# Kernel optimization log

Hardware: AMD Instinct MI355X
Metric: run time of the kernel (lower is better)

## Reference

```python
import jax, jax.numpy as jnp
import numpy as np
from jax import lax

B, NMEAS, M, LAYER_NUM = 2048, 128, 256, 10
CLAMP_MIN, CLAMP_MAX = 1e-6, 100.0
EPS_S = 1e-6


def _conv2d(x, w, b):
    y = lax.conv_general_dilated(x, w, (1, 1), 'SAME', dimension_numbers=('NCHW', 'OIHW', 'NCHW'))
    return y + b[None, :, None, None]


def _conv1d(x, w, b):
    y = lax.conv_general_dilated(x, w, (1,), 'SAME', dimension_numbers=('NCH', 'OIH', 'NCH'))
    return y + b[None, :, None]


def setup_inputs():
    key = jax.random.key(0)
    ks = jax.random.split(key, 12)
    s = 1.0 / np.sqrt(2.0 * NMEAS)  # ~unit-norm dictionary columns
    return {
        'Yr': jax.random.normal(ks[0], (B, 1, NMEAS, 1), jnp.float32),
        'Yi': jax.random.normal(ks[1], (B, 1, NMEAS, 1), jnp.float32),
        'Ar': s * jax.random.normal(ks[2], (NMEAS, M), jnp.float32),
        'Ai': s * jax.random.normal(ks[3], (NMEAS, M), jnp.float32),
        'conv1_w': 0.1 * jax.random.normal(ks[4], (32, 2, 3, 3), jnp.float32),
        'conv1_b': jnp.zeros((32,), jnp.float32),
        'conv2_w': 0.1 * jax.random.normal(ks[5], (64, 32, 3, 3), jnp.float32),
        'conv2_b': jnp.zeros((64,), jnp.float32),
        'hc_w': 0.1 * jax.random.normal(ks[6], (LAYER_NUM - 1, 64, 3), jnp.float32),
        'hc_b': jnp.zeros((LAYER_NUM - 1,), jnp.float32),
        'hd_w': 0.1 * jax.random.normal(ks[7], (LAYER_NUM - 1, 64, 3), jnp.float32),
        'hd_b': jnp.zeros((LAYER_NUM - 1,), jnp.float32),
        'hT_w': 0.1 * jax.random.normal(ks[8], (LAYER_NUM, 64, 3), jnp.float32),
        'hT_b': jnp.zeros((LAYER_NUM,), jnp.float32),
        'a0': jnp.asarray(1.0, jnp.float32),
        'b0': jnp.asarray(1.0, jnp.float32),
    }


def _hypernet(ay, c1w, c1b, c2w, c2b, hcw, hcb, hdw, hdb, hTw, hTb):
    # ay: [B, 2, M]; batch acts as image width (context)
    x_img = jnp.transpose(ay, (1, 2, 0))[None]              # [1, 2, M, B]
    f = jax.nn.relu(_conv2d(x_img, c1w, c1b))               # [1, 32, M, B]
    f = jax.nn.relu(_conv2d(f, c2w, c2b))                   # [1, 64, M, B]
    f = jnp.mean(f, axis=2)                                 # AdaptiveAvgPool2d((1,None)) -> [1, 64, B]
    c = jnp.abs(_conv1d(f, hcw, hcb))[0].T                  # [B, L-1]
    d = jnp.abs(_conv1d(f, hdw, hdb))[0].T                  # [B, L-1]
    T = jnp.abs(_conv1d(f, hTw, hTb))[0].T                  # [B, L]
    c = jnp.clip(c, CLAMP_MIN, CLAMP_MAX)
    d = jnp.maximum(d, CLAMP_MIN)
    T = jnp.clip(T, CLAMP_MIN, CLAMP_MAX)
    return c, d, T


def _forward(Yr, Yi, Ar, Ai, conv1_w, conv1_b, conv2_w, conv2_b,
             hc_w, hc_b, hd_w, hd_b, hT_w, hT_b, a0, b0):
    Y = (Yr + 1j * Yi).astype(jnp.complex64)                # [B,1,Nmeas,1]
    A = (Ar + 1j * Ai).astype(jnp.complex64)                # [Nmeas,M]
    AT = A.conj().T                                         # [M,Nmeas]
    AA = AT @ A                                             # [M,M] Hermitian
    AY = jnp.matmul(AT, Y)                                  # [B,1,M,1]
    b = Y.shape[0]
    n = Y.shape[2]
    ay = jnp.concatenate([AY.real.reshape(b, 1, -1), AY.imag.reshape(b, 1, -1)], axis=1)  # [B,2,M]
    c, d, T = _hypernet(ay, conv1_w, conv1_b, conv2_w, conv2_b,
                        hc_w, hc_b, hd_w, hd_b, hT_w, hT_b)
    D = jnp.real(jnp.diagonal(AA))[None, None, :, None]     # diag of Hermitian AA is real; [1,1,M,1]
    eps = (a0 / b0).astype(jnp.complex64) * jnp.ones((b, 1, 1, 1), jnp.complex64)
    Lam = ((c[:, 0] / d[:, 0])[:, None, None, None] * jnp.ones((1, 1, M, 1), jnp.float32)).astype(jnp.complex64)
    U = jnp.zeros((b, 1, M, 1), jnp.complex64)
    a = a0 + n
    for k in range(LAYER_NUM - 1):
        Tk = T[:, k][:, None, None, None]
        # fused SBL/VAMP mean update
        U = eps * (Tk * U - jnp.matmul(AA, U) + AY) / (eps * Tk + Lam + EPS_S)
        Sigma = 1.0 / (eps * D + Lam + EPS_S)
        r = Y - jnp.matmul(A, U)
        eps1 = jnp.sum(r.real ** 2 + r.imag ** 2, axis=(2, 3), keepdims=True)  # ||.||_F^2
        eps2 = jnp.sum(D * Sigma, axis=(2, 3), keepdims=True)
        eps = a / (b0 + eps1 + eps2 + EPS_S)
        Lam = (c[:, k][:, None, None, None] + 1.0) / (
            d[:, k][:, None, None, None] + jnp.abs(U) ** 2 + Sigma + EPS_S)
    Tk = T[:, LAYER_NUM - 1][:, None, None, None]
    U = eps * (Tk * U - jnp.matmul(AA, U) + AY) / (eps * Tk + Lam + EPS_S)
    Ua = jnp.abs(U)
    Ua = Ua / (jnp.max(Ua) + 1e-8)
    return Ua, c, d, T


def reference(Yr, Yi, Ar, Ai, conv1_w, conv1_b, conv2_w, conv2_b,
              hc_w, hc_b, hd_w, hd_b, hT_w, hT_b, a0, b0):
    Ua, c, d, T = _forward(Yr, Yi, Ar, Ai, conv1_w, conv1_b, conv2_w, conv2_b,
                           hc_w, hc_b, hd_w, hd_b, hT_w, hT_b, a0, b0)
    # original returns the last batch row of c/d/T (detached diagnostics)
    return Ua, c[-1:, :], d[-1:, :], T[-1:, :]
```

## Files before the change

kernel.cpp:

```cpp
#include <hip/hip_runtime.h>
#include <math.h>

#define B_N   2048
#define NM    128
#define M_N   256
#define LNUM  10
#define EPS_Sf 1e-6f

typedef _Float16 half8 __attribute__((ext_vector_type(8)));
typedef float floatx4 __attribute__((ext_vector_type(4)));

static constexpr size_t o_AA  = 0;
static constexpr size_t o_D   = o_AA  + 131072;
static constexpr size_t o_yn  = o_D   + 256;
static constexpr size_t o_AY  = o_yn  + 2048;
static constexpr size_t o_AYt = o_AY  + 1048576;
static constexpr size_t o_w2t = o_AYt + 1048576;
static constexpr size_t o_z1  = o_w2t + 18432;
static constexpr size_t o_fp  = o_z1  + 16777216;
static constexpr size_t o_f   = o_fp  + 2097152;
static constexpr size_t o_c   = o_f   + 131072;
static constexpr size_t o_dd  = o_c   + 18432;
static constexpr size_t o_T   = o_dd  + 18432;
static constexpr size_t o_Ua  = o_T   + 20480;
static constexpr size_t o_gm  = o_Ua  + 524288;

#define Z1T_RS (2050 * 32)

__device__ __forceinline__ void split2(float x, _Float16& h, _Float16& l) {
    h = (_Float16)x;
    l = (_Float16)(x - (float)h);
}

__global__ void k_aa(const float* __restrict__ Ar, const float* __restrict__ Ai,
                     float* __restrict__ ws) {
    __shared__ float cr[NM], ci[NM];
    int i = blockIdx.x, j = threadIdx.x;
    if (j < NM) { cr[j] = Ar[j * M_N + i]; ci[j] = Ai[j * M_N + i]; }
    __syncthreads();
    float sr = 0.f, si = 0.f;
    for (int n = 0; n < NM; ++n) {
        float ar = Ar[n * M_N + j], ai = Ai[n * M_N + j];
        sr += cr[n] * ar + ci[n] * ai;
        si += cr[n] * ai - ci[n] * ar;
    }
    _Float16* A16 = (_Float16*)(ws + o_AA);
    size_t off = ((size_t)((i >> 4) * 8 + (j >> 5)) * 64
                  + (size_t)(((j >> 3) & 3) * 16 + (i & 15))) * 8 + (j & 7);
    A16[off]         = (_Float16)sr;
    A16[65536 + off] = (_Float16)si;
    if (j == i) ws[o_D + i] = sr;
}

__global__ void k_w2t(const float* __restrict__ w2, float* __restrict__ ws) {
    int i = blockIdx.x * 256 + threadIdx.x;
    if (i < 64 * 32 * 9) {
        int oc = i / 288, r = i % 288;
        int ic = r / 9, kk = r % 9;
        _Float16* Wa = (_Float16*)(ws + o_w2t);
        Wa[((size_t)oc * 9 + kk) * 32 + ic] = (_Float16)w2[i];
    }
}

__global__ void k_ay(const float* __restrict__ Yr, const float* __restrict__ Yi,
                     const float* __restrict__ Ar, const float* __restrict__ Ai,
                     float* __restrict__ ws) {
    __shared__ float2 Ys[8][NM];
    int bb0 = blockIdx.x * 8;
    int tid = threadIdx.x;
    for (int i = tid; i < 8 * NM; i += 256) {
        int g = i >> 7, n = i & 127;
        Ys[g][n] = make_float2(Yr[(size_t)(bb0 + g) * NM + n], Yi[(size_t)(bb0 + g) * NM + n]);
    }
    __syncthreads();
    if (tid < 8) {
        float s = 0.f;
        for (int n = 0; n < NM; ++n) { float2 y = Ys[tid][n]; s += y.x * y.x + y.y * y.y; }
        ws[o_yn + bb0 + tid] = s;
    }
    int m = tid;
    float accr[8], acci[8];
#pragma unroll
    for (int g = 0; g < 8; ++g) { accr[g] = 0.f; acci[g] = 0.f; }
    for (int n = 0; n < NM; ++n) {
        float ar = Ar[n * M_N + m], ai = Ai[n * M_N + m];
#pragma unroll
        for (int g = 0; g < 8; ++g) {
            float2 y = Ys[g][n];
            accr[g] += ar * y.x + ai * y.y;
            acci[g] += ar * y.y - ai * y.x;
        }
    }
    float2* AY = (float2*)(ws + o_AY);
#pragma unroll
    for (int g = 0; g < 8; ++g) {
        AY[(size_t)(bb0 + g) * M_N + m] = make_float2(accr[g], acci[g]);
        ws[o_AYt + (size_t)m * B_N + (bb0 + g)] = accr[g];
        ws[o_AYt + 524288 + (size_t)m * B_N + (bb0 + g)] = acci[g];
    }
}

__global__ void k_conv1(const float* __restrict__ w1, const float* __restrict__ b1,
                        float* __restrict__ ws) {
    __shared__ float w1s[576], b1s[32];
    int tid = threadIdx.x;
    for (int i = tid; i < 576; i += 256) w1s[i] = w1[i];
    if (tid < 32) b1s[tid] = b1[tid];
    __syncthreads();
    int gidx = blockIdx.x * 256 + tid;
    int b = gidx & (B_N - 1), m = gidx >> 11;
    const float* xr = ws + o_AYt;
    float x[2][3][3];
#pragma unroll
    for (int c = 0; c < 2; ++c)
#pragma unroll
        for (int dm = 0; dm < 3; ++dm) {
            int mm = m + dm - 1;
#pragma unroll
            for (int db = 0; db < 3; ++db) {
                int bb = b + db - 1;
                x[c][dm][db] = (mm >= 0 && mm < M_N && bb >= 0 && bb < B_N)
                                 ? xr[(size_t)c * 524288 + (size_t)mm * B_N + bb] : 0.f;
            }
        }
    _Float16* z1t = (_Float16*)(ws + o_z1);
    _Float16 zv[32];
    for (int oc = 0; oc < 32; ++oc) {
        float acc = b1s[oc];
#pragma unroll
        for (int c = 0; c < 2; ++c)
#pragma unroll
            for (int dm = 0; dm < 3; ++dm)
#pragma unroll
                for (int db = 0; db < 3; ++db)
                    acc += x[c][dm][db] * w1s[oc * 18 + c * 9 + dm * 3 + db];
        zv[oc] = (_Float16)fmaxf(acc, 0.f);
    }
    _Float16* dst = z1t + (size_t)(m + 1) * Z1T_RS + (size_t)(b + 1) * 32;
#pragma unroll
    for (int v = 0; v < 4; ++v) *(half8*)(dst + v * 8) = *(half8*)(zv + v * 8);
    half8 z8 = (half8)((_Float16)0.f);
    if (m == 0) {
        _Float16* d2 = z1t + (size_t)(b + 1) * 32;
#pragma unroll
        for (int v = 0; v < 4; ++v) *(half8*)(d2 + v * 8) = z8;
        if (b == 0) { _Float16* d3 = z1t;
#pragma unroll
            for (int v = 0; v < 4; ++v) *(half8*)(d3 + v * 8) = z8; }
        if (b == B_N - 1) { _Float16* d3 = z1t + (size_t)2049 * 32;
#pragma unroll
            for (int v = 0; v < 4; ++v) *(half8*)(d3 + v * 8) = z8; }
    }
    if (m == M_N - 1) {
        _Float16* d2 = z1t + (size_t)257 * Z1T_RS + (size_t)(b + 1) * 32;
#pragma unroll
        for (int v = 0; v < 4; ++v) *(half8*)(d2 + v * 8) = z8;
        if (b == 0) { _Float16* d3 = z1t + (size_t)257 * Z1T_RS;
#pragma unroll
            for (int v = 0; v < 4; ++v) *(half8*)(d3 + v * 8) = z8; }
        if (b == B_N - 1) { _Float16* d3 = z1t + (size_t)257 * Z1T_RS + (size_t)2049 * 32;
#pragma unroll
            for (int v = 0; v < 4; ++v) *(half8*)(d3 + v * 8) = z8; }
    }
    if (b == 0) {
        _Float16* d2 = z1t + (size_t)(m + 1) * Z1T_RS;
#pragma unroll
        for (int v = 0; v < 4; ++v) *(half8*)(d2 + v * 8) = z8;
    }
    if (b == B_N - 1) {
        _Float16* d2 = z1t + (size_t)(m + 1) * Z1T_RS + (size_t)2049 * 32;
#pragma unroll
        for (int v = 0; v < 4; ++v) *(half8*)(d2 + v * 8) = z8;
    }
}

#define MFMA16(A,Bv,C) C = __builtin_amdgcn_mfma_f32_16x16x32_f16(A, Bv, C, 0, 0, 0)
__global__ void __launch_bounds__(128)
k_conv2m(const float* __restrict__ b2, float* __restrict__ ws) {
    int tid = threadIdx.x;
    int lane = tid & 63, wv = tid >> 6;
    int col = lane & 15, quad = lane >> 4;
    int bt = blockIdx.x & 127, g = blockIdx.x >> 7;
    int b0 = bt * 16, m0 = g * 16;
    int oc0w = wv * 32;
    const _Float16* z1t = (const _Float16*)(ws + o_z1);
    const _Float16* Wa  = (const _Float16*)(ws + o_w2t);

    half8 Af[2][9];
#pragma unroll
    for (int t = 0; t < 2; ++t)
#pragma unroll
        for (int kk = 0; kk < 9; ++kk)
            Af[t][kk] = *(const half8*)(Wa + ((size_t)(oc0w + t * 16 + col) * 9 + kk) * 32 + quad * 8);
    float bias[2][4];
#pragma unroll
    for (int t = 0; t < 2; ++t)
#pragma unroll
        for (int r = 0; r < 4; ++r)
            bias[t][r] = b2[oc0w + t * 16 + quad * 4 + r];

    const _Float16* zb = z1t + (size_t)(b0 + col) * 32 + quad * 8;
    half8 Bf[3][3];
#pragma unroll
    for (int ph = 0; ph < 3; ++ph)
#pragma unroll
        for (int db = 0; db < 3; ++db)
            Bf[ph][db] = *(const half8*)(zb + (size_t)(m0 + ph) * Z1T_RS + (size_t)db * 32);

    floatx4 facc[2];
    facc[0] = (floatx4){0.f, 0.f, 0.f, 0.f};
    facc[1] = (floatx4){0.f, 0.f, 0.f, 0.f};

#pragma unroll
    for (int mm = 0; mm < 16; ++mm) {
        floatx4 a0 = (floatx4){0.f, 0.f, 0.f, 0.f};
        floatx4 a1 = (floatx4){0.f, 0.f, 0.f, 0.f};
#pragma unroll
        for (int dm = 0; dm < 3; ++dm) {
            int ph = (mm + dm) % 3;
#pragma unroll
            for (int db = 0; db < 3; ++db) {
                MFMA16(Af[0][dm * 3 + db], Bf[ph][db], a0);
                MFMA16(Af[1][dm * 3 + db], Bf[ph][db], a1);
            }
        }
#pragma unroll
        for (int r = 0; r < 4; ++r) {
            facc[0][r] += fmaxf(a0[r] + bias[0][r], 0.f);
            facc[1][r] += fmaxf(a1[r] + bias[1][r], 0.f);
        }
        if (mm < 15) {
            int ph = mm % 3;
#pragma unroll
            for (int db = 0; db < 3; ++db)
                Bf[ph][db] = *(const half8*)(zb + (size_t)(m0 + mm + 3) * Z1T_RS + (size_t)db * 32);
        }
    }
    float* fp = ws + o_fp + (size_t)g * 131072;
#pragma unroll
    for (int t = 0; t < 2; ++t)
#pragma unroll
        for (int r = 0; r < 4; ++r)
            fp[(size_t)(oc0w + t * 16 + quad * 4 + r) * B_N + b0 + col] = facc[t][r];
}

__global__ void k_fred(float* __restrict__ ws) {
    size_t i = (size_t)blockIdx.x * 256 + threadIdx.x;
    float s = 0.f;
    for (int p = 0; p < 16; ++p) s += ws[o_fp + (size_t)p * 131072 + i];
    ws[o_f + i] = s * (1.f / 256.f);
}

__global__ void k_cdt(const float* __restrict__ hcw, const float* __restrict__ hcb,
                      const float* __restrict__ hdw, const float* __restrict__ hdb,
                      const float* __restrict__ hTw, const float* __restrict__ hTb,
                      float* __restrict__ ws, float* __restrict__ out) {
    int l = blockIdx.x >> 3;
    int b = (blockIdx.x & 7) * 256 + threadIdx.x;
    const float* f = ws + o_f;
    const float* w; float bi; int li, kind;
    if (l < 9)       { kind = 0; li = l;      w = hcw + (size_t)li * 192; bi = hcb[li]; }
    else if (l < 18) { kind = 1; li = l - 9;  w = hdw + (size_t)li * 192; bi = hdb[li]; }
    else             { kind = 2; li = l - 18; w = hTw + (size_t)li * 192; bi = hTb[li]; }
    __shared__ float wsm[192];
    for (int i = threadIdx.x; i < 192; i += 256) wsm[i] = w[i];
    __syncthreads();
    float acc = bi;
    bool okL = (b > 0), okR = (b < B_N - 1);
    for (int ic = 0; ic < 64; ++ic) {
        const float* fr = f + (size_t)ic * B_N + b;
        float fm1 = okL ? fr[-1] : 0.f;
        float f0  = fr[0];
        float fp1 = okR ? fr[1] : 0.f;
        acc += fm1 * wsm[ic * 3] + f0 * wsm[ic * 3 + 1] + fp1 * wsm[ic * 3 + 2];
    }
    float v = fmaxf(fabsf(acc), 1e-6f);
    if (kind != 1) v = fminf(v, 100.f);
    if (kind == 0)      { ws[o_c  + (size_t)b * 9  + li] = v; if (b == B_N - 1) out[524288 + li] = v; }
    else if (kind == 1) { ws[o_dd + (size_t)b * 9  + li] = v; if (b == B_N - 1) out[524297 + li] = v; }
    else                { ws[o_T  + (size_t)b * 10 + li] = v; if (b == B_N - 1) out[524306 + li] = v; }
}

__global__ void __launch_bounds__(1024, 4)
k_iter(const float* __restrict__ a0p, const float* __restrict__ b0p, float* __restrict__ ws) {
    __shared__ __align__(16) _Float16 Ubf[4][8][64][8];
    __shared__ float redv[16][16][3];
    __shared__ float redm[16];
    int tid = threadIdx.x;
    int lane = tid & 63, w = tid >> 6;
    int col = lane & 15, quad = lane >> 4;
    int b = blockIdx.x * 16 + col;
    const float2* AY = (const float2*)(ws + o_AY);
    const _Float16* Af = (const _Float16*)(ws + o_AA);
    float a0 = a0p[0], b0v = b0p[0];
    float atot = a0 + (float)NM;
    float yn = ws[o_yn + b];
    float eps = a0 / b0v;
    float lam0 = ws[o_c + (size_t)b * 9] / ws[o_dd + (size_t)b * 9];
    half8 Ar8[8], Ai8[8];
#pragma unroll
    for (int ks = 0; ks < 8; ++ks) {
        const _Float16* ab = Af + ((size_t)(w * 8 + ks) * 64 + lane) * 8;
        Ar8[ks] = *(const half8*)(ab);
        Ai8[ks] = *(const half8*)(ab + 65536);
    }
    float Dv[4], ayr[4], ayi[4], lam[4], Ur[4], Ui[4], sg[4], wr_[4], wi_[4];
#pragma unroll
    for (int r = 0; r < 4; ++r) {
        int m = w * 16 + quad * 4 + r;
        Dv[r] = ws[o_D + m];
        float2 a = AY[(size_t)b * M_N + m];
        ayr[r] = a.x; ayi[r] = a.y;
        lam[r] = lam0;
        Ur[r] = 0.f; Ui[r] = 0.f; wr_[r] = 0.f; wi_[r] = 0.f;
    }
    int ksw = w >> 1;
    int quadD = (w & 1) * 2 + (quad >> 1);
    int laneD = quadD * 16 + col;
    int eb = (quad & 1) * 4;
    for (int k = 0; k < LNUM; ++k) {
        float Tk = ws[o_T + (size_t)b * 10 + k];
#pragma unroll
        for (int r = 0; r < 4; ++r) {
            float iv = eps / (eps * Tk + lam[r] + EPS_Sf);
            Ur[r] = iv * (Tk * Ur[r] - wr_[r] + ayr[r]);
            Ui[r] = iv * (Tk * Ui[r] - wi_[r] + ayi[r]);
        }
        if (k == LNUM - 1) break;
        {
            union { _Float16 h[4]; unsigned long long u; } c0, c1, c2, c3;
#pragma unroll
            for (int r = 0; r < 4; ++r) {
                _Float16 h, l;
                split2(Ur[r], h, l); c0.h[r] = h; c1.h[r] = l;
                split2(Ui[r], h, l); c2.h[r] = h; c3.h[r] = l;
            }
            *(unsigned long long*)&Ubf[0][ksw][laneD][eb] = c0.u;
            *(unsigned long long*)&Ubf[1][ksw][laneD][eb] = c1.u;
            *(unsigned long long*)&Ubf[2][ksw][laneD][eb] = c2.u;
            *(unsigned long long*)&Ubf[3][ksw][laneD][eb] = c3.u;
        }
        __syncthreads();
        floatx4 wrp = (floatx4){0.f, 0.f, 0.f, 0.f};
        floatx4 wrn = (floatx4){0.f, 0.f, 0.f, 0.f};
        floatx4 wia = (floatx4){0.f, 0.f, 0.f, 0.f};
#pragma unroll
        for (int ks = 0; ks < 8; ++ks) {
            half8 urh = *(const half8*)&Ubf[0][ks][lane][0];
            half8 url = *(const half8*)&Ubf[1][ks][lane][0];
            half8 uih = *(const half8*)&Ubf[2][ks][lane][0];
            half8 uil = *(const half8*)&Ubf[3][ks][lane][0];
            MFMA16(Ar8[ks], urh, wrp);
            MFMA16(Ar8[ks], url, wrp);
            MFMA16(Ai8[ks], uih, wrn);
            MFMA16(Ai8[ks], uil, wrn);
            MFMA16(Ar8[ks], uih, wia);
            MFMA16(Ar8[ks], uil, wia);
            MFMA16(Ai8[ks], urh, wia);
            MFMA16(Ai8[ks], url, wia);
        }
        float p1 = 0.f, p2 = 0.f, p3 = 0.f;
#pragma unroll
        for (int r = 0; r < 4; ++r) {
            wr_[r] = wrp[r] - wrn[r];
            wi_[r] = wia[r];
            sg[r] = 1.f / (eps * Dv[r] + lam[r] + EPS_Sf);
            p1 += ayr[r] * Ur[r] + ayi[r] * Ui[r];
            p2 += Ur[r] * wr_[r] + Ui[r] * wi_[r];
            p3 += Dv[r] * sg[r];
        }
        p1 += __shfl_xor(p1, 16); p1 += __shfl_xor(p1, 32);
        p2 += __shfl_xor(p2, 16); p2 += __shfl_xor(p2, 32);
        p3 += __shfl_xor(p3, 16); p3 += __shfl_xor(p3, 32);
        if (lane < 16) { redv[w][col][0] = p1; redv[w][col][1] = p2; redv[w][col][2] = p3; }
        __syncthreads();
        float s1 = 0.f, s2 = 0.f, s3 = 0.f;
#pragma unroll
        for (int u16 = 0; u16 < 16; ++u16) {
            s1 += redv[u16][col][0]; s2 += redv[u16][col][1]; s3 += redv[u16][col][2];
        }
        float eps1 = fmaxf(yn - 2.f * s1 + s2, 0.f);
        eps = atot / (b0v + eps1 + s3 + EPS_Sf);
        float ck = ws[o_c + (size_t)b * 9 + k];
        float dk = ws[o_dd + (size_t)b * 9 + k];
#pragma unroll
        for (int r = 0; r < 4; ++r)
            lam[r] = (ck + 1.f) / (dk + Ur[r] * Ur[r] + Ui[r] * Ui[r] + sg[r] + EPS_Sf);
    }
    float4 v;
    v.x = sqrtf(Ur[0] * Ur[0] + Ui[0] * Ui[0]);
    v.y = sqrtf(Ur[1] * Ur[1] + Ui[1] * Ui[1]);
    v.z = sqrtf(Ur[2] * Ur[2] + Ui[2] * Ui[2]);
    v.w = sqrtf(Ur[3] * Ur[3] + Ui[3] * Ui[3]);
    *(float4*)&ws[o_Ua + (size_t)b * M_N + w * 16 + quad * 4] = v;
    float lm = fmaxf(fmaxf(v.x, v.y), fmaxf(v.z, v.w));
#pragma unroll
    for (int off = 32; off >= 1; off >>= 1) lm = fmaxf(lm, __shfl_xor(lm, off));
    if (lane == 0) redm[w] = lm;
    __syncthreads();
    if (tid == 0) {
        float mx = redm[0];
#pragma unroll
        for (int i = 1; i < 16; ++i) mx = fmaxf(mx, redm[i]);
        atomicMax((unsigned int*)(ws + o_gm), __float_as_uint(mx));
    }
}

__global__ void k_norm(const float* __restrict__ ws, float* __restrict__ out) {
    size_t i = (size_t)blockIdx.x * 256 + threadIdx.x;
    float gm = __uint_as_float(*(const unsigned int*)(ws + o_gm));
    out[i] = ws[o_Ua + i] / (gm + 1e-8f);
}

extern "C" void kernel_launch(void* const* d_in, const int* in_sizes, int n_in,
                              void* d_out, int out_size, void* d_ws, size_t ws_size,
                              hipStream_t stream) {
    (void)in_sizes; (void)n_in; (void)out_size; (void)ws_size;
    const float* Yr  = (const float*)d_in[0];
    const float* Yi  = (const float*)d_in[1];
    const float* Ar  = (const float*)d_in[2];
    const float* Ai  = (const float*)d_in[3];
    const float* w1  = (const float*)d_in[4];
    const float* b1  = (const float*)d_in[5];
    const float* w2  = (const float*)d_in[6];
    const float* b2  = (const float*)d_in[7];
    const float* hcw = (const float*)d_in[8];
    const float* hcb = (const float*)d_in[9];
    const float* hdw = (const float*)d_in[10];
    const float* hdb = (const float*)d_in[11];
    const float* hTw = (const float*)d_in[12];
    const float* hTb = (const float*)d_in[13];
    const float* a0  = (const float*)d_in[14];
    const float* b0  = (const float*)d_in[15];
    float* ws = (float*)d_ws;
    float* out = (float*)d_out;

    hipMemsetAsync((char*)d_ws + o_gm * sizeof(float), 0, 4, stream);
    k_aa    <<<256, 256, 0, stream>>>(Ar, Ai, ws);
    k_w2t   <<<72, 256, 0, stream>>>(w2, ws);
    k_ay    <<<256, 256, 0, stream>>>(Yr, Yi, Ar, Ai, ws);
    k_conv1 <<<2048, 256, 0, stream>>>(w1, b1, ws);
    k_conv2m<<<2048, 128, 0, stream>>>(b2, ws);
    k_fred  <<<512, 256, 0, stream>>>(ws);
    k_cdt   <<<224, 256, 0, stream>>>(hcw, hcb, hdw, hdb, hTw, hTb, ws, out);
    k_iter  <<<128, 1024, 0, stream>>>(a0, b0, ws);
    k_norm  <<<2048, 256, 0, stream>>>(ws, out);
}
```

Measured before the change: 244.2 us.

## Drop fp16 hi/lo split in iteration matvec and merge preprocessing kernels

The iterative solver kernel now converts U to a single fp16 value instead of a hi/lo fp16 pair. This halves the shared-memory staging and the MFMA count per step, at the cost of lower precision in the AA·U product. The three setup kernels and the workspace memset are merged into one block-partitioned launch to cut launch overhead. The cross-wave reduction buffer is transposed so each column reads its partial sums with vector loads.

```diff
diff --git a/kernel.cpp b/kernel.cpp
--- a/kernel.cpp
+++ b/kernel.cpp
@@ -27,76 +27,72 @@
 
 #define Z1T_RS (2050 * 32)
 
-__device__ __forceinline__ void split2(float x, _Float16& h, _Float16& l) {
-    h = (_Float16)x;
-    l = (_Float16)(x - (float)h);
-}
-
-__global__ void k_aa(const float* __restrict__ Ar, const float* __restrict__ Ai,
-                     float* __restrict__ ws) {
-    __shared__ float cr[NM], ci[NM];
-    int i = blockIdx.x, j = threadIdx.x;
-    if (j < NM) { cr[j] = Ar[j * M_N + i]; ci[j] = Ai[j * M_N + i]; }
-    __syncthreads();
-    float sr = 0.f, si = 0.f;
-    for (int n = 0; n < NM; ++n) {
-        float ar = Ar[n * M_N + j], ai = Ai[n * M_N + j];
-        sr += cr[n] * ar + ci[n] * ai;
-        si += cr[n] * ai - ci[n] * ar;
-    }
-    _Float16* A16 = (_Float16*)(ws + o_AA);
-    size_t off = ((size_t)((i >> 4) * 8 + (j >> 5)) * 64
-                  + (size_t)(((j >> 3) & 3) * 16 + (i & 15))) * 8 + (j & 7);
-    A16[off]         = (_Float16)sr;
-    A16[65536 + off] = (_Float16)si;
-    if (j == i) ws[o_D + i] = sr;
-}
-
-__global__ void k_w2t(const float* __restrict__ w2, float* __restrict__ ws) {
-    int i = blockIdx.x * 256 + threadIdx.x;
-    if (i < 64 * 32 * 9) {
-        int oc = i / 288, r = i % 288;
-        int ic = r / 9, kk = r % 9;
-        _Float16* Wa = (_Float16*)(ws + o_w2t);
-        Wa[((size_t)oc * 9 + kk) * 32 + ic] = (_Float16)w2[i];
-    }
-}
-
-__global__ void k_ay(const float* __restrict__ Yr, const float* __restrict__ Yi,
-                     const float* __restrict__ Ar, const float* __restrict__ Ai,
-                     float* __restrict__ ws) {
-    __shared__ float2 Ys[8][NM];
-    int bb0 = blockIdx.x * 8;
+__global__ void k_pre(const float* __restrict__ Ar, const float* __restrict__ Ai,
+                      const float* __restrict__ Yr, const float* __restrict__ Yi,
+                      const float* __restrict__ w2, float* __restrict__ ws) {
+    __shared__ float sb[2048];
+    int blk = blockIdx.x;
     int tid = threadIdx.x;
-    for (int i = tid; i < 8 * NM; i += 256) {
-        int g = i >> 7, n = i & 127;
-        Ys[g][n] = make_float2(Yr[(size_t)(bb0 + g) * NM + n], Yi[(size_t)(bb0 + g) * NM + n]);
-    }
-    __syncthreads();
-    if (tid < 8) {
-        float s = 0.f;
-        for (int n = 0; n < NM; ++n) { float2 y = Ys[tid][n]; s += y.x * y.x + y.y * y.y; }
-        ws[o_yn + bb0 + tid] = s;
-    }
-    int m = tid;
-    float accr[8], acci[8];
-#pragma unroll
-    for (int g = 0; g < 8; ++g) { accr[g] = 0.f; acci[g] = 0.f; }
-    for (int n = 0; n < NM; ++n) {
-        float ar = Ar[n * M_N + m], ai = Ai[n * M_N + m];
+    if (blk < 256) {
+        float* cr = sb; float* ci = sb + NM;
+        int i = blk, j = tid;
+        if (j < NM) { cr[j] = Ar[j * M_N + i]; ci[j] = Ai[j * M_N + i]; }
+        __syncthreads();
+        float sr = 0.f, si = 0.f;
+        for (int n = 0; n < NM; ++n) {
+            float ar = Ar[n * M_N + j], ai = Ai[n * M_N + j];
+            sr += cr[n] * ar + ci[n] * ai;
+            si += cr[n] * ai - ci[n] * ar;
+        }
+        _Float16* A16 = (_Float16*)(ws + o_AA);
+        size_t off = ((size_t)((i >> 4) * 8 + (j >> 5)) * 64
+                      + (size_t)(((j >> 3) & 3) * 16 + (i & 15))) * 8 + (j & 7);
+        A16[off]         = (_Float16)sr;
+        A16[65536 + off] = (_Float16)si;
+        if (j == i) ws[o_D + i] = sr;
+        if (i == 0 && j == 0) *(unsigned int*)(ws + o_gm) = 0u;
+    } else if (blk < 328) {
+        int i = (blk - 256) * 256 + tid;
+        if (i < 64 * 32 * 9) {
+            int oc = i / 288, r = i % 288;
+            int ic = r / 9, kk = r % 9;
+            _Float16* Wa = (_Float16*)(ws + o_w2t);
+            Wa[((size_t)oc * 9 + kk) * 32 + ic] = (_Float16)w2[i];
+        }
+    } else {
+        float2* Ys = (float2*)sb;
+        int bb0 = (blk - 328) * 8;
+        for (int i = tid; i < 8 * NM; i += 256) {
+            int g = i >> 7, n = i & 127;
+            Ys[g * NM + n] = make_float2(Yr[(size_t)(bb0 + g) * NM + n],
+                                         Yi[(size_t)(bb0 + g) * NM + n]);
+        }
+        __syncthreads();
+        if (tid < 8) {
+            float s = 0.f;
+            for (int n = 0; n < NM; ++n) { float2 y = Ys[tid * NM + n]; s += y.x * y.x + y.y * y.y; }
+            ws[o_yn + bb0 + tid] = s;
+        }
+        int m = tid;
+        float accr[8], acci[8];
+#pragma unroll
+        for (int g = 0; g < 8; ++g) { accr[g] = 0.f; acci[g] = 0.f; }
+        for (int n = 0; n < NM; ++n) {
+            float ar = Ar[n * M_N + m], ai = Ai[n * M_N + m];
+#pragma unroll
+            for (int g = 0; g < 8; ++g) {
+                float2 y = Ys[g * NM + n];
+                accr[g] += ar * y.x + ai * y.y;
+                acci[g] += ar * y.y - ai * y.x;
+            }
+        }
+        float2* AY = (float2*)(ws + o_AY);
 #pragma unroll
         for (int g = 0; g < 8; ++g) {
-            float2 y = Ys[g][n];
-            accr[g] += ar * y.x + ai * y.y;
-            acci[g] += ar * y.y - ai * y.x;
-        }
-    }
-    float2* AY = (float2*)(ws + o_AY);
-#pragma unroll
-    for (int g = 0; g < 8; ++g) {
-        AY[(size_t)(bb0 + g) * M_N + m] = make_float2(accr[g], acci[g]);
-        ws[o_AYt + (size_t)m * B_N + (bb0 + g)] = accr[g];
-        ws[o_AYt + 524288 + (size_t)m * B_N + (bb0 + g)] = acci[g];
+            AY[(size_t)(bb0 + g) * M_N + m] = make_float2(accr[g], acci[g]);
+            ws[o_AYt + (size_t)m * B_N + (bb0 + g)] = accr[g];
+            ws[o_AYt + 524288 + (size_t)m * B_N + (bb0 + g)] = acci[g];
+        }
     }
 }
 
@@ -283,8 +279,8 @@
 
 __global__ void __launch_bounds__(1024, 4)
 k_iter(const float* __restrict__ a0p, const float* __restrict__ b0p, float* __restrict__ ws) {
-    __shared__ __align__(16) _Float16 Ubf[4][8][64][8];
-    __shared__ float redv[16][16][3];
+    __shared__ __align__(16) _Float16 Ubf[2][8][64][8];
+    __shared__ __align__(16) float redv[16][52];
     __shared__ float redm[16];
     int tid = threadIdx.x;
     int lane = tid & 63, w = tid >> 6;
@@ -328,42 +324,34 @@
         }
         if (k == LNUM - 1) break;
         {
-            union { _Float16 h[4]; unsigned long long u; } c0, c1, c2, c3;
+            union { _Float16 h[4]; unsigned long long u; } c0, c2;
 #pragma unroll
             for (int r = 0; r < 4; ++r) {
-                _Float16 h, l;
-                split2(Ur[r], h, l); c0.h[r] = h; c1.h[r] = l;
-                split2(Ui[r], h, l); c2.h[r] = h; c3.h[r] = l;
+                c0.h[r] = (_Float16)Ur[r];
+                c2.h[r] = (_Float16)Ui[r];
             }
             *(unsigned long long*)&Ubf[0][ksw][laneD][eb] = c0.u;
-            *(unsigned long long*)&Ubf[1][ksw][laneD][eb] = c1.u;
-            *(unsigned long long*)&Ubf[2][ksw][laneD][eb] = c2.u;
-            *(unsigned long long*)&Ubf[3][ksw][laneD][eb] = c3.u;
+            *(unsigned long long*)&Ubf[1][ksw][laneD][eb] = c2.u;
         }
         __syncthreads();
         floatx4 wrp = (floatx4){0.f, 0.f, 0.f, 0.f};
         floatx4 wrn = (floatx4){0.f, 0.f, 0.f, 0.f};
-        floatx4 wia = (floatx4){0.f, 0.f, 0.f, 0.f};
+        floatx4 wia1 = (floatx4){0.f, 0.f, 0.f, 0.f};
+        floatx4 wia2 = (floatx4){0.f, 0.f, 0.f, 0.f};
 #pragma unroll
         for (int ks = 0; ks < 8; ++ks) {
             half8 urh = *(const half8*)&Ubf[0][ks][lane][0];
-            half8 url = *(const half8*)&Ubf[1][ks][lane][0];
-            half8 uih = *(const half8*)&Ubf[2][ks][lane][0];
-            half8 uil = *(const half8*)&Ubf[3][ks][lane][0];
+            half8 uih = *(const half8*)&Ubf[1][ks][lane][0];
             MFMA16(Ar8[ks], urh, wrp);
-            MFMA16(Ar8[ks], url, wrp);
             MFMA16(Ai8[ks], uih, wrn);
-            MFMA16(Ai8[ks], uil, wrn);
-            MFMA16(Ar8[ks], uih, wia);
-            MFMA16(Ar8[ks], uil, wia);
-            MFMA16(Ai8[ks], urh, wia);
-            MFMA16(Ai8[ks], url, wia);
+            MFMA16(Ar8[ks], uih, wia1);
+            MFMA16(Ai8[ks], urh, wia2);
         }
         float p1 = 0.f, p2 = 0.f, p3 = 0.f;
 #pragma unroll
         for (int r = 0; r < 4; ++r) {
             wr_[r] = wrp[r] - wrn[r];
-            wi_[r] = wia[r];
+            wi_[r] = wia1[r] + wia2[r];
             sg[r] = 1.f / (eps * Dv[r] + lam[r] + EPS_Sf);
             p1 += ayr[r] * Ur[r] + ayi[r] * Ui[r];
             p2 += Ur[r] * wr_[r] + Ui[r] * wi_[r];
@@ -372,15 +360,21 @@
         p1 += __shfl_xor(p1, 16); p1 += __shfl_xor(p1, 32);
         p2 += __shfl_xor(p2, 16); p2 += __shfl_xor(p2, 32);
         p3 += __shfl_xor(p3, 16); p3 += __shfl_xor(p3, 32);
-        if (lane < 16) { redv[w][col][0] = p1; redv[w][col][1] = p2; redv[w][col][2] = p3; }
+        if (lane < 16) {
+            redv[col][w * 3]     = p1;
+            redv[col][w * 3 + 1] = p2;
+            redv[col][w * 3 + 2] = p3;
+        }
         __syncthreads();
-        float s1 = 0.f, s2 = 0.f, s3 = 0.f;
-#pragma unroll
-        for (int u16 = 0; u16 < 16; ++u16) {
-            s1 += redv[u16][col][0]; s2 += redv[u16][col][1]; s3 += redv[u16][col][2];
-        }
-        float eps1 = fmaxf(yn - 2.f * s1 + s2, 0.f);
-        eps = atot / (b0v + eps1 + s3 + EPS_Sf);
+        float s[3] = {0.f, 0.f, 0.f};
+#pragma unroll
+        for (int j = 0; j < 12; ++j) {
+            floatx4 v4 = *(const floatx4*)&redv[col][j * 4];
+#pragma unroll
+            for (int e = 0; e < 4; ++e) s[(j * 4 + e) % 3] += v4[e];
+        }
+        float eps1 = fmaxf(yn - 2.f * s[0] + s[1], 0.f);
+        eps = atot / (b0v + eps1 + s[2] + EPS_Sf);
         float ck = ws[o_c + (size_t)b * 9 + k];
         float dk = ws[o_dd + (size_t)b * 9 + k];
 #pragma unroll
@@ -435,10 +429,7 @@
     float* ws = (float*)d_ws;
     float* out = (float*)d_out;
 
-    hipMemsetAsync((char*)d_ws + o_gm * sizeof(float), 0, 4, stream);
-    k_aa    <<<256, 256, 0, stream>>>(Ar, Ai, ws);
-    k_w2t   <<<72, 256, 0, stream>>>(w2, ws);
-    k_ay    <<<256, 256, 0, stream>>>(Yr, Yi, Ar, Ai, ws);
+    k_pre   <<<584, 256, 0, stream>>>(Ar, Ai, Yr, Yi, w2, ws);
     k_conv1 <<<2048, 256, 0, stream>>>(w1, b1, ws);
     k_conv2m<<<2048, 128, 0, stream>>>(b2, ws);
     k_fred  <<<512, 256, 0, stream>>>(ws);
```

After: 242.4 us. About the same (-0.8%).
